# Optimization experiments

Hardware: AMD Instinct MI355X
Metric: run time of the kernel (lower is better)

The kernel has to match this reference:

```python
import jax, jax.numpy as jnp
import numpy as np

B, S, D, H = 2, 2048, 1024, 16
DK = D // H

def setup_inputs() -> dict:
    key = jax.random.key(0)
    ks = jax.random.split(key, 5)
    scale = 1.0 / np.sqrt(D)
    return {
        "query": jax.random.normal(ks[0], (B, S, D), dtype=jnp.float32),
        "mask": jnp.ones((B, S, S), dtype=jnp.int32),
        "Wq": jax.random.normal(ks[1], (D, D), dtype=jnp.float32) * scale,
        "bq": jnp.zeros((D,), dtype=jnp.float32),
        "Wk": jax.random.normal(ks[2], (D, D), dtype=jnp.float32) * scale,
        "bk": jnp.zeros((D,), dtype=jnp.float32),
        "Wv": jax.random.normal(ks[3], (D, D), dtype=jnp.float32) * scale,
        "bv": jnp.zeros((D,), dtype=jnp.float32),
        "Wo": jax.random.normal(ks[4], (D, D), dtype=jnp.float32) * scale,
        "bo": jnp.zeros((D,), dtype=jnp.float32),
    }

def reference(query, mask, Wq, bq, Wk, bk, Wv, bv, Wo, bo):
    # self-attention: key = value = query (torch Linear: x @ W.T + b)
    b, s, d = query.shape
    def proj(x, W, bias):
        y = jnp.einsum('bsd,ed->bse', x, W) + bias
        return y.reshape(b, s, H, DK).transpose(0, 2, 1, 3)  # [B,H,S,DK]
    q = proj(query, Wq, bq)
    k = proj(query, Wk, bk)
    v = proj(query, Wv, bv)
    scores = jnp.einsum('bhqd,bhkd->bhqk', q, k) / jnp.sqrt(jnp.float32(DK))
    m = mask[:, None, :, :]  # [B,1,S,S] (torch unsqueeze(1) for 3D mask)
    scores = jnp.where(m == 0, jnp.float32(-1e9), scores)
    w = jax.nn.softmax(scores, axis=-1)  # dropout: eval mode -> identity
    o = jnp.einsum('bhqk,bhkd->bhqd', w, v)
    o = o.transpose(0, 2, 1, 3).reshape(b, s, d)
    return jnp.einsum('bsd,ed->bse', o, Wo) + bo
```

## Files before the change

kernel.cpp:

```cpp
#include <hip/hip_runtime.h>


typedef _Float16 f16x8 __attribute__((ext_vector_type(8)));
typedef _Float16 f16x4 __attribute__((ext_vector_type(4)));
typedef _Float16 f16x2 __attribute__((ext_vector_type(2)));
typedef float    f32x4 __attribute__((ext_vector_type(4)));
typedef float    f32x16 __attribute__((ext_vector_type(16)));
typedef int      i32x4 __attribute__((ext_vector_type(4)));
typedef unsigned u32x2 __attribute__((ext_vector_type(2)));

#define MFMA32(a, b, c) __builtin_amdgcn_mfma_f32_32x32x16_f16(a, b, c, 0, 0, 0)
#define MFMA16(a, b, c) __builtin_amdgcn_mfma_f32_16x16x32_f16(a, b, c, 0, 0, 0)

#if __has_builtin(__builtin_amdgcn_exp2f)
#define EXP2(x) __builtin_amdgcn_exp2f(x)
#else
#define EXP2(x) exp2f(x)
#endif

__device__ __forceinline__ void gld16(const void* g, void* l) {
    __builtin_amdgcn_global_load_lds(
        (const __attribute__((address_space(1))) void*)g,
        (__attribute__((address_space(3))) void*)l, 16, 0, 0);
}

__device__ __forceinline__ void conv1k(const float* __restrict__ in,
                                       _Float16* __restrict__ out, int base) {
    const int i = base + threadIdx.x * 4;
    float4 v = *(const float4*)(in + i);
    f16x4 o;
    o.x = (_Float16)v.x; o.y = (_Float16)v.y; o.z = (_Float16)v.z; o.w = (_Float16)v.w;
    *(f16x4*)(out + i) = o;
}

__global__ void k_pre(const float* __restrict__ X, const float* __restrict__ Wq,
                      const float* __restrict__ Wk, const float* __restrict__ Wv,
                      const float* __restrict__ Wo,
                      _Float16* __restrict__ Xh, _Float16* __restrict__ Wqh,
                      _Float16* __restrict__ Wkh, _Float16* __restrict__ Wvh,
                      _Float16* __restrict__ Woh, int* __restrict__ flag) {
    const int bid = blockIdx.x;
    if (bid == 0 && threadIdx.x == 0) *flag = 0;
    if (bid < 4096)      conv1k(X,  Xh,  bid * 1024);
    else if (bid < 5120) conv1k(Wq, Wqh, (bid - 4096) * 1024);
    else if (bid < 6144) conv1k(Wk, Wkh, (bid - 5120) * 1024);
    else if (bid < 7168) conv1k(Wv, Wvh, (bid - 6144) * 1024);
    else                 conv1k(Wo, Woh, (bid - 7168) * 1024);
}

__global__ __launch_bounds__(256, 3) void k_qkv(
    const _Float16* __restrict__ X,
    const _Float16* __restrict__ Wqh, const _Float16* __restrict__ Wkh,
    const _Float16* __restrict__ Wvh,
    const float* __restrict__ bq, const float* __restrict__ bk,
    const float* __restrict__ bv,
    _Float16* __restrict__ Qo, _Float16* __restrict__ Ko, _Float16* __restrict__ Vo,
    const int* __restrict__ mask, int* __restrict__ flag)
{
    __shared__ _Float16 SH[128 * 136];
    const int tid = threadIdx.x;

    if (blockIdx.x >= 24) {
        const int sb = (blockIdx.x - 24) + 8 * blockIdx.y;
        const int4* m4 = (const int4*)mask + (size_t)sb * 8192 + tid;
        int bad = 0;
#pragma unroll 4
        for (int i = 0; i < 32; ++i) {
            int4 v = m4[i * 256];
            bad |= (v.x == 0) | (v.y == 0) | (v.z == 0) | (v.w == 0);
        }
        if (bad) atomicOr(flag, 1);
        return;
    }

    _Float16* As = SH;
    _Float16* Bs = SH + 128 * 64;
    const int lane = tid & 63, wv = tid >> 6;
    const int wrow = wv >> 1, wcol = wv & 1;
    const int l5 = lane & 31, half = lane >> 5;
    const int which = blockIdx.x >> 3;
    const _Float16* W   = which == 0 ? Wqh : which == 1 ? Wkh : Wvh;
    const float*   bias = which == 0 ? bq  : which == 1 ? bk  : bv;
    const int n0 = (blockIdx.x & 7) * 128;
    const int m0 = blockIdx.y * 128;

    f32x16 acc[2][2];
#pragma unroll
    for (int a = 0; a < 2; ++a)
#pragma unroll
        for (int bb = 0; bb < 2; ++bb)
#pragma unroll
            for (int r = 0; r < 16; ++r) acc[a][bb][r] = 0.f;

#pragma unroll 1
    for (int k0 = 0; k0 < 1024; k0 += 64) {
        __syncthreads();
#pragma unroll
        for (int it = 0; it < 4; ++it) {
            const int wbase = it * 256 + wv * 64;
            const int ci = wbase + lane;
            const int r = ci >> 3;
            const int c8 = (((ci & 7) ^ (r & 7)) * 8);
            gld16(X + (size_t)(m0 + r) * 1024 + k0 + c8, As + wbase * 8);
            gld16(W + (size_t)(n0 + r) * 1024 + k0 + c8, Bs + wbase * 8);
        }
        __syncthreads();
#pragma unroll
        for (int ks = 0; ks < 4; ++ks) {
            f16x8 af[2], bf[2];
#pragma unroll
            for (int mt = 0; mt < 2; ++mt)
                af[mt] = *(const f16x8*)(As + (wrow * 64 + mt * 32 + l5) * 64 +
                                         (((ks * 2 + half) ^ (l5 & 7)) * 8));
#pragma unroll
            for (int nt = 0; nt < 2; ++nt)
                bf[nt] = *(const f16x8*)(Bs + (wcol * 64 + nt * 32 + l5) * 64 +
                                         (((ks * 2 + half) ^ (l5 & 7)) * 8));
#pragma unroll
            for (int mt = 0; mt < 2; ++mt)
#pragma unroll
                for (int nt = 0; nt < 2; ++nt)
                    acc[mt][nt] = MFMA32(af[mt], bf[nt], acc[mt][nt]);
        }
    }

    __syncthreads();
    const int b_ = m0 >> 11;
    const int s_base = m0 & 2047;
    if (which == 2) {
#pragma unroll
        for (int nt = 0; nt < 2; ++nt) {
            const int e_l = wcol * 64 + nt * 32 + l5;
            const float bv_ = bias[n0 + e_l];
#pragma unroll
            for (int mt = 0; mt < 2; ++mt)
#pragma unroll
                for (int g = 0; g < 4; ++g) {
                    const int m_l = wrow * 64 + mt * 32 + 8 * g + 4 * half;
                    f16x4 pk;
#pragma unroll
                    for (int j = 0; j < 4; ++j)
                        pk[j] = (_Float16)(acc[mt][nt][4 * g + j] + bv_);
                    *(f16x4*)(SH + e_l * 136 + m_l) = pk;
                }
        }
        __syncthreads();
#pragma unroll
        for (int p = 0; p < 8; ++p) {
            const int e_l = p * 16 + (tid >> 4);
            const int s8 = (tid & 15) * 8;
            f16x8 vv = *(const f16x8*)(SH + e_l * 136 + s8);
            const int e = n0 + e_l;
            const int h = e >> 6, dk = e & 63;
            const int s0 = s_base + s8;
            const size_t idx = ((((size_t)(b_ * 16 + h) * 128 + (s0 >> 4)) * 2 +
                                (dk >> 5)) * 64 + (dk & 31) + 32 * ((s8 >> 3) & 1)) * 8;
            *(f16x8*)(Vo + idx) = vv;
        }
    } else {
        const float qs = (which == 0) ? 0.18033688011112042f : 1.0f;
#pragma unroll
        for (int nt = 0; nt < 2; ++nt) {
            const int e_l = wcol * 64 + nt * 32 + l5;
            const float bv_ = bias[n0 + e_l];
#pragma unroll
            for (int mt = 0; mt < 2; ++mt)
#pragma unroll
                for (int r = 0; r < 16; ++r) {
                    const int m_l = wrow * 64 + mt * 32 + (r & 3) + 8 * (r >> 2) + 4 * half;
                    SH[m_l * 136 + e_l] = (_Float16)((acc[mt][nt][r] + bv_) * qs);
                }
        }
        __syncthreads();
#pragma unroll
        for (int p = 0; p < 8; ++p) {
            const int m_l = p * 16 + (tid >> 4);
            const int c8 = (tid & 15) * 8;
            f16x8 vv = *(const f16x8*)(SH + m_l * 136 + c8);
            const int e = n0 + c8;
            const int h = e >> 6, dk = e & 63;
            const int s = s_base + m_l;
            if (which == 0) {
                *(f16x8*)(Qo + (((size_t)b_ * 16 + h) * 2048 + s) * 64 + dk) = vv;
            } else {
                const size_t idx = ((((size_t)(b_ * 16 + h) * 64 + (s >> 5)) * 4 +
                                    (dk >> 4)) * 64 + (s & 31) + 32 * ((dk >> 3) & 1)) * 8;
                *(f16x8*)(Ko + idx) = vv;
            }
        }
    }
}

__global__ __launch_bounds__(256, 4) void k_oproj(
    const _Float16* __restrict__ Oin, const _Float16* __restrict__ Woh,
    const float* __restrict__ bo, float* __restrict__ out)
{
    __shared__ _Float16 As[128 * 64];
    __shared__ _Float16 Bs[64 * 64];
    const int tid = threadIdx.x;
    const int lane = tid & 63, wv = tid >> 6;
    const int quad = lane >> 4, lc = lane & 15;
    const int n0 = blockIdx.x * 64;
    const int m0 = blockIdx.y * 128;

    const f32x4 fzero = {0.f, 0.f, 0.f, 0.f};
    f32x4 acc[2][4];
#pragma unroll
    for (int a = 0; a < 2; ++a)
#pragma unroll
        for (int bb = 0; bb < 4; ++bb) acc[a][bb] = fzero;

#pragma unroll 1
    for (int k0 = 0; k0 < 1024; k0 += 64) {
        __syncthreads();
#pragma unroll
        for (int it = 0; it < 4; ++it) {
            const int ci = it * 256 + tid;
            const int r = ci >> 3;
            const int c8 = (((ci & 7) ^ (r & 7)) * 8);
            gld16(Oin + (size_t)(m0 + r) * 1024 + k0 + c8, As + ci * 8);
        }
#pragma unroll
        for (int it = 0; it < 2; ++it) {
            const int ci = it * 256 + tid;
            const int r = ci >> 3;
            const int c8 = (((ci & 7) ^ (r & 7)) * 8);
            gld16(Woh + (size_t)(n0 + r) * 1024 + k0 + c8, Bs + ci * 8);
        }
        __syncthreads();
#pragma unroll
        for (int ks = 0; ks < 2; ++ks) {
            f16x8 af[2], bf[4];
#pragma unroll
            for (int mt = 0; mt < 2; ++mt)
                af[mt] = *(const f16x8*)(As + (wv * 32 + mt * 16 + lc) * 64 +
                                         (((ks * 4 + quad) ^ (lc & 7)) * 8));
#pragma unroll
            for (int nt = 0; nt < 4; ++nt)
                bf[nt] = *(const f16x8*)(Bs + (nt * 16 + lc) * 64 +
                                         (((ks * 4 + quad) ^ (lc & 7)) * 8));
#pragma unroll
            for (int mt = 0; mt < 2; ++mt)
#pragma unroll
                for (int nt = 0; nt < 4; ++nt)
                    acc[mt][nt] = MFMA16(af[mt], bf[nt], acc[mt][nt]);
        }
    }
#pragma unroll
    for (int nt = 0; nt < 4; ++nt) {
        const int e = n0 + nt * 16 + lc;
        const float bv_ = bo[e];
#pragma unroll
        for (int mt = 0; mt < 2; ++mt)
#pragma unroll
            for (int i = 0; i < 4; ++i) {
                const int m = m0 + wv * 32 + mt * 16 + quad * 4 + i;
                out[(size_t)m * 1024 + e] = acc[mt][nt][i] + bv_;
            }
    }
}

__global__ __launch_bounds__(256, 4) void k_attn(
    const _Float16* __restrict__ Q, const _Float16* __restrict__ Kp,
    const _Float16* __restrict__ Vp, const int* __restrict__ mask,
    const int* __restrict__ flag, _Float16* __restrict__ O)
{
    __shared__ float Os[2][32 * 64];
    __shared__ float Ls[2][32];

    const int tid = threadIdx.x;
    const int lane = tid & 63, wv = tid >> 6;
    const int l5 = lane & 31, half = lane >> 5;
    const int qt = wv >> 1, kh = wv & 1;
    const int bh = blockIdx.x;
    const int b = bh >> 4, h = bh & 15;
    const int qb = blockIdx.y * 64 + qt * 32;
    const int phase = (bh & 3) * 8;

    const _Float16* Qb = Q  + (size_t)bh * 2048 * 64;
    const _Float16* Kb = Kp + (size_t)bh * 131072;
    const _Float16* Vb = Vp + (size_t)bh * 131072;

    f16x8 qf[4];
#pragma unroll
    for (int kk = 0; kk < 4; ++kk)
        qf[kk] = *(const f16x8*)(Qb + (size_t)(qb + l5) * 64 + kk * 16 + half * 8);

    const f16x2 one2 = {(_Float16)1.f, (_Float16)1.f};

    f32x16 o[2];
#pragma unroll
    for (int nt = 0; nt < 2; ++nt)
#pragma unroll
        for (int r = 0; r < 16; ++r) o[nt][r] = 0.f;
    float l_i = 0.f;

    const bool has_zero = (*flag != 0);

    f16x8 kf[4];
    {
        const int kb0 = kh * 32 + phase;
#pragma unroll
        for (int kk = 0; kk < 4; ++kk)
            kf[kk] = *(const f16x8*)(Kb + ((size_t)(kb0 * 4 + kk) * 64 + lane) * 8);
    }

#pragma unroll 2
    for (int it = 0; it < 32; ++it) {
        const int kb = kh * 32 + ((it + phase) & 31);
        f16x8 vf[4];
#pragma unroll
        for (int ks = 0; ks < 2; ++ks)
#pragma unroll
            for (int nt = 0; nt < 2; ++nt)
                vf[ks * 2 + nt] = *(const f16x8*)(Vb +
                    ((size_t)((kb * 2 + ks) * 2 + nt) * 64 + lane) * 8);

        f32x16 st;
#pragma unroll
        for (int r = 0; r < 16; ++r) st[r] = 0.f;
        __builtin_amdgcn_s_setprio(1);
        st = MFMA32(kf[0], qf[0], st);
        st = MFMA32(kf[1], qf[1], st);
        st = MFMA32(kf[2], qf[2], st);
        st = MFMA32(kf[3], qf[3], st);
        __builtin_amdgcn_s_setprio(0);

        {
            const int nkb = kh * 32 + ((it + 1 + phase) & 31);
#pragma unroll
            for (int kk = 0; kk < 4; ++kk)
                kf[kk] = *(const f16x8*)(Kb + ((size_t)(nkb * 4 + kk) * 64 + lane) * 8);
        }

        if (has_zero) {
            const int q = qb + l5;
            const int* mr = mask + ((size_t)b * 2048 + q) * 2048 + kb * 32;
            for (int r = 0; r < 16; ++r) {
                const int kk_ = (r & 3) + 8 * (r >> 2) + 4 * half;
                if (mr[kk_] == 0) st[r] = -1e30f;
            }
        }

        unsigned u[8];
        float rs = 0.f;
#pragma unroll
        for (int j = 0; j < 8; ++j) {
            const float p0 = EXP2(st[2 * j]);
            const float p1 = EXP2(st[2 * j + 1]);
            u[j] = __builtin_bit_cast(unsigned, __builtin_amdgcn_cvt_pkrtz(p0, p1));
#if __has_builtin(__builtin_amdgcn_fdot2)
            rs = __builtin_amdgcn_fdot2(__builtin_bit_cast(f16x2, u[j]), one2, rs, false);
#else
            rs += p0 + p1;
#endif
        }
        rs += __shfl_xor(rs, 32);
        l_i += rs;

        u32x2 r02 = __builtin_amdgcn_permlane32_swap(u[0], u[2], false, false);
        u32x2 r13 = __builtin_amdgcn_permlane32_swap(u[1], u[3], false, false);
        u32x2 r46 = __builtin_amdgcn_permlane32_swap(u[4], u[6], false, false);
        u32x2 r57 = __builtin_amdgcn_permlane32_swap(u[5], u[7], false, false);
        i32x4 a0 = { (int)r02[0], (int)r13[0], (int)r02[1], (int)r13[1] };
        i32x4 a1 = { (int)r46[0], (int)r57[0], (int)r46[1], (int)r57[1] };
        f16x8 pa0 = __builtin_bit_cast(f16x8, a0);
        f16x8 pa1 = __builtin_bit_cast(f16x8, a1);

        __builtin_amdgcn_s_setprio(1);
        o[0] = MFMA32(pa0, vf[0], o[0]);
        o[1] = MFMA32(pa0, vf[1], o[1]);
        o[0] = MFMA32(pa1, vf[2], o[0]);
        o[1] = MFMA32(pa1, vf[3], o[1]);
        __builtin_amdgcn_s_setprio(0);
    }

    if (kh == 1) {
        if (half == 0) Ls[qt][l5] = l_i;
#pragma unroll
        for (int nt = 0; nt < 2; ++nt)
#pragma unroll
            for (int r = 0; r < 16; ++r) {
                const int q_loc = (r & 3) + 8 * (r >> 2) + 4 * half;
                Os[qt][q_loc * 64 + nt * 32 + l5] = o[nt][r];
            }
    }
    __syncthreads();
    if (kh == 0) {
        const float linv = 1.f / (l_i + Ls[qt][l5]);
#pragma unroll
        for (int r = 0; r < 16; ++r) {
            const int q_loc = (r & 3) + 8 * (r >> 2) + 4 * half;
            const float lv = __shfl(linv, q_loc);
            const int q = qb + q_loc;
            _Float16* orow = O + ((size_t)b * 2048 + q) * 1024 + h * 64;
#pragma unroll
            for (int nt = 0; nt < 2; ++nt) {
                const float val = o[nt][r] + Os[qt][q_loc * 64 + nt * 32 + l5];
                orow[nt * 32 + l5] = (_Float16)(val * lv);
            }
        }
    }
}

extern "C" void kernel_launch(void* const* d_in, const int* in_sizes, int n_in,
                              void* d_out, int out_size, void* d_ws, size_t ws_size,
                              hipStream_t stream) {
    const float* query = (const float*)d_in[0];
    const int*   mask  = (const int*)d_in[1];
    const float* Wq = (const float*)d_in[2]; const float* bq = (const float*)d_in[3];
    const float* Wk = (const float*)d_in[4]; const float* bk = (const float*)d_in[5];
    const float* Wv = (const float*)d_in[6]; const float* bv = (const float*)d_in[7];
    const float* Wo = (const float*)d_in[8]; const float* bo = (const float*)d_in[9];
    float* out = (float*)d_out;

    char* ws = (char*)d_ws;
    _Float16* Xh  = (_Float16*)(ws);
    _Float16* Wqh = (_Float16*)(ws + 8388608);
    _Float16* Wkh = (_Float16*)(ws + 10485760);
    _Float16* Wvh = (_Float16*)(ws + 12582912);
    _Float16* Woh = (_Float16*)(ws + 14680064);
    _Float16* Qh  = (_Float16*)(ws + 16777216);
    _Float16* Kh  = (_Float16*)(ws + 25165824);
    _Float16* Vh  = (_Float16*)(ws + 33554432);
    _Float16* Oh  = Xh;
    int* flag     = (int*)(ws + 41943040);

    k_pre<<<8192, 256, 0, stream>>>(query, Wq, Wk, Wv, Wo,
                                    Xh, Wqh, Wkh, Wvh, Woh, flag);
    k_qkv<<<dim3(32, 32), 256, 0, stream>>>(Xh, Wqh, Wkh, Wvh, bq, bk, bv,
                                            Qh, Kh, Vh, mask, flag);
    k_attn<<<dim3(32, 32), 256, 0, stream>>>(Qh, Kh, Vh, mask, flag, Oh);
    k_oproj<<<dim3(16, 32), 256, 0, stream>>>(Oh, Woh, bo, out);
}
```

Measured before the change: 207.7 us.

## Software-pipeline attention loop so QK^T of next block overlaps softmax of current

Restructures the key-block loop into a two-stage software pipeline. The QK^T MFMAs for block i+1 are issued before the exp/pack/PV work of block i, with the S tiles ping-ponging between two registers. The aim is to hide MFMA latency behind the VALU softmax work and the permlane shuffles. In exchange it uses more registers (two score tiles live at once) and an unroll-1 loop over 16 double-steps, which may reduce occupancy.

```diff
diff --git a/kernel.cpp b/kernel.cpp
--- a/kernel.cpp
+++ b/kernel.cpp
@@ -304,75 +304,152 @@
         for (int kk = 0; kk < 4; ++kk)
             kf[kk] = *(const f16x8*)(Kb + ((size_t)(kb0 * 4 + kk) * 64 + lane) * 8);
     }
-
-#pragma unroll 2
-    for (int it = 0; it < 32; ++it) {
-        const int kb = kh * 32 + ((it + phase) & 31);
+    f32x16 st0;
+#pragma unroll
+    for (int r = 0; r < 16; ++r) st0[r] = 0.f;
+    st0 = MFMA32(kf[0], qf[0], st0);
+    st0 = MFMA32(kf[1], qf[1], st0);
+    st0 = MFMA32(kf[2], qf[2], st0);
+    st0 = MFMA32(kf[3], qf[3], st0);
+    {
+        const int kb1 = kh * 32 + ((1 + phase) & 31);
+#pragma unroll
+        for (int kk = 0; kk < 4; ++kk)
+            kf[kk] = *(const f16x8*)(Kb + ((size_t)(kb1 * 4 + kk) * 64 + lane) * 8);
+    }
+
+#pragma unroll 1
+    for (int it = 0; it < 16; ++it) {
+        const int kbA = kh * 32 + ((2 * it + phase) & 31);
+        const int kbB = kh * 32 + ((2 * it + 1 + phase) & 31);
+        const int kbC = kh * 32 + ((2 * it + 2 + phase) & 31);
+        const int kbD = kh * 32 + ((2 * it + 3 + phase) & 31);
+
         f16x8 vf[4];
 #pragma unroll
         for (int ks = 0; ks < 2; ++ks)
 #pragma unroll
             for (int nt = 0; nt < 2; ++nt)
                 vf[ks * 2 + nt] = *(const f16x8*)(Vb +
-                    ((size_t)((kb * 2 + ks) * 2 + nt) * 64 + lane) * 8);
-
-        f32x16 st;
-#pragma unroll
-        for (int r = 0; r < 16; ++r) st[r] = 0.f;
+                    ((size_t)((kbA * 2 + ks) * 2 + nt) * 64 + lane) * 8);
+
+        f32x16 st1;
+#pragma unroll
+        for (int r = 0; r < 16; ++r) st1[r] = 0.f;
         __builtin_amdgcn_s_setprio(1);
-        st = MFMA32(kf[0], qf[0], st);
-        st = MFMA32(kf[1], qf[1], st);
-        st = MFMA32(kf[2], qf[2], st);
-        st = MFMA32(kf[3], qf[3], st);
+        st1 = MFMA32(kf[0], qf[0], st1);
+        st1 = MFMA32(kf[1], qf[1], st1);
+        st1 = MFMA32(kf[2], qf[2], st1);
+        st1 = MFMA32(kf[3], qf[3], st1);
         __builtin_amdgcn_s_setprio(0);
 
-        {
-            const int nkb = kh * 32 + ((it + 1 + phase) & 31);
-#pragma unroll
-            for (int kk = 0; kk < 4; ++kk)
-                kf[kk] = *(const f16x8*)(Kb + ((size_t)(nkb * 4 + kk) * 64 + lane) * 8);
-        }
+#pragma unroll
+        for (int kk = 0; kk < 4; ++kk)
+            kf[kk] = *(const f16x8*)(Kb + ((size_t)(kbC * 4 + kk) * 64 + lane) * 8);
 
         if (has_zero) {
             const int q = qb + l5;
-            const int* mr = mask + ((size_t)b * 2048 + q) * 2048 + kb * 32;
+            const int* mr = mask + ((size_t)b * 2048 + q) * 2048 + kbA * 32;
             for (int r = 0; r < 16; ++r) {
                 const int kk_ = (r & 3) + 8 * (r >> 2) + 4 * half;
-                if (mr[kk_] == 0) st[r] = -1e30f;
-            }
-        }
-
-        unsigned u[8];
-        float rs = 0.f;
-#pragma unroll
-        for (int j = 0; j < 8; ++j) {
-            const float p0 = EXP2(st[2 * j]);
-            const float p1 = EXP2(st[2 * j + 1]);
-            u[j] = __builtin_bit_cast(unsigned, __builtin_amdgcn_cvt_pkrtz(p0, p1));
+                if (mr[kk_] == 0) st0[r] = -1e30f;
+            }
+        }
+
+        {
+            unsigned u[8];
+            float rs = 0.f;
+#pragma unroll
+            for (int j = 0; j < 8; ++j) {
+                const float p0 = EXP2(st0[2 * j]);
+                const float p1 = EXP2(st0[2 * j + 1]);
+                u[j] = __builtin_bit_cast(unsigned, __builtin_amdgcn_cvt_pkrtz(p0, p1));
 #if __has_builtin(__builtin_amdgcn_fdot2)
-            rs = __builtin_amdgcn_fdot2(__builtin_bit_cast(f16x2, u[j]), one2, rs, false);
+                rs = __builtin_amdgcn_fdot2(__builtin_bit_cast(f16x2, u[j]), one2, rs, false);
 #else
-            rs += p0 + p1;
+                rs += p0 + p1;
 #endif
-        }
-        rs += __shfl_xor(rs, 32);
-        l_i += rs;
-
-        u32x2 r02 = __builtin_amdgcn_permlane32_swap(u[0], u[2], false, false);
-        u32x2 r13 = __builtin_amdgcn_permlane32_swap(u[1], u[3], false, false);
-        u32x2 r46 = __builtin_amdgcn_permlane32_swap(u[4], u[6], false, false);
-        u32x2 r57 = __builtin_amdgcn_permlane32_swap(u[5], u[7], false, false);
-        i32x4 a0 = { (int)r02[0], (int)r13[0], (int)r02[1], (int)r13[1] };
-        i32x4 a1 = { (int)r46[0], (int)r57[0], (int)r46[1], (int)r57[1] };
-        f16x8 pa0 = __builtin_bit_cast(f16x8, a0);
-        f16x8 pa1 = __builtin_bit_cast(f16x8, a1);
-
+            }
+            rs += __shfl_xor(rs, 32);
+            l_i += rs;
+            u32x2 r02 = __builtin_amdgcn_permlane32_swap(u[0], u[2], false, false);
+            u32x2 r13 = __builtin_amdgcn_permlane32_swap(u[1], u[3], false, false);
+            u32x2 r46 = __builtin_amdgcn_permlane32_swap(u[4], u[6], false, false);
+            u32x2 r57 = __builtin_amdgcn_permlane32_swap(u[5], u[7], false, false);
+            i32x4 a0 = { (int)r02[0], (int)r13[0], (int)r02[1], (int)r13[1] };
+            i32x4 a1 = { (int)r46[0], (int)r57[0], (int)r46[1], (int)r57[1] };
+            f16x8 pa0 = __builtin_bit_cast(f16x8, a0);
+            f16x8 pa1 = __builtin_bit_cast(f16x8, a1);
+
+            __builtin_amdgcn_s_setprio(1);
+            o[0] = MFMA32(pa0, vf[0], o[0]);
+            o[1] = MFMA32(pa0, vf[1], o[1]);
+            o[0] = MFMA32(pa1, vf[2], o[0]);
+            o[1] = MFMA32(pa1, vf[3], o[1]);
+            __builtin_amdgcn_s_setprio(0);
+        }
+
+#pragma unroll
+        for (int ks = 0; ks < 2; ++ks)
+#pragma unroll
+            for (int nt = 0; nt < 2; ++nt)
+                vf[ks * 2 + nt] = *(const f16x8*)(Vb +
+                    ((size_t)((kbB * 2 + ks) * 2 + nt) * 64 + lane) * 8);
+
+#pragma unroll
+        for (int r = 0; r < 16; ++r) st0[r] = 0.f;
         __builtin_amdgcn_s_setprio(1);
-        o[0] = MFMA32(pa0, vf[0], o[0]);
-        o[1] = MFMA32(pa0, vf[1], o[1]);
-        o[0] = MFMA32(pa1, vf[2], o[0]);
-        o[1] = MFMA32(pa1, vf[3], o[1]);
+        st0 = MFMA32(kf[0], qf[0], st0);
+        st0 = MFMA32(kf[1], qf[1], st0);
+        st0 = MFMA32(kf[2], qf[2], st0);
+        st0 = MFMA32(kf[3], qf[3], st0);
         __builtin_amdgcn_s_setprio(0);
+
+#pragma unroll
+        for (int kk = 0; kk < 4; ++kk)
+            kf[kk] = *(const f16x8*)(Kb + ((size_t)(kbD * 4 + kk) * 64 + lane) * 8);
+
+        if (has_zero) {
+            const int q = qb + l5;
+            const int* mr = mask + ((size_t)b * 2048 + q) * 2048 + kbB * 32;
+            for (int r = 0; r < 16; ++r) {
+                const int kk_ = (r & 3) + 8 * (r >> 2) + 4 * half;
+                if (mr[kk_] == 0) st1[r] = -1e30f;
+            }
+        }
+
+        {
+            unsigned u[8];
+            float rs = 0.f;
+#pragma unroll
+            for (int j = 0; j < 8; ++j) {
+                const float p0 = EXP2(st1[2 * j]);
+                const float p1 = EXP2(st1[2 * j + 1]);
+                u[j] = __builtin_bit_cast(unsigned, __builtin_amdgcn_cvt_pkrtz(p0, p1));
+#if __has_builtin(__builtin_amdgcn_fdot2)
+                rs = __builtin_amdgcn_fdot2(__builtin_bit_cast(f16x2, u[j]), one2, rs, false);
+#else
+                rs += p0 + p1;
+#endif
+            }
+            rs += __shfl_xor(rs, 32);
+            l_i += rs;
+            u32x2 r02 = __builtin_amdgcn_permlane32_swap(u[0], u[2], false, false);
+            u32x2 r13 = __builtin_amdgcn_permlane32_swap(u[1], u[3], false, false);
+            u32x2 r46 = __builtin_amdgcn_permlane32_swap(u[4], u[6], false, false);
+            u32x2 r57 = __builtin_amdgcn_permlane32_swap(u[5], u[7], false, false);
+            i32x4 a0 = { (int)r02[0], (int)r13[0], (int)r02[1], (int)r13[1] };
+            i32x4 a1 = { (int)r46[0], (int)r57[0], (int)r46[1], (int)r57[1] };
+            f16x8 pb0 = __builtin_bit_cast(f16x8, a0);
+            f16x8 pb1 = __builtin_bit_cast(f16x8, a1);
+
+            __builtin_amdgcn_s_setprio(1);
+            o[0] = MFMA32(pb0, vf[0], o[0]);
+            o[1] = MFMA32(pb0, vf[1], o[1]);
+            o[0] = MFMA32(pb1, vf[2], o[0]);
+            o[1] = MFMA32(pb1, vf[3], o[1]);
+            __builtin_amdgcn_s_setprio(0);
+        }
     }
 
     if (kh == 1) {
```

Measured after the change: 238.5 us. 14.8% more time.
